# Kernel optimization log

Measured on AMD Instinct MI355X. Metric: run time of the kernel, lower is better.

The kernel has to match this reference:

```python
import jax, jax.numpy as jnp
import numpy as np

E = 5          # number of experts / candidate encoders
NSUB = 13      # subband axis from x.reshape([B, 13, -1])


def _complex_corr_mean(y, y_):
    # y: [E, B, 13, F] (interleaved re/im), y_: [B, 13, F]
    ai, aj = y[..., 0::2], y[..., 1::2]        # [E,B,13,F/2]
    bi, bj = y_[..., 0::2], y_[..., 1::2]      # [B,13,F/2]
    i = (ai * bi + aj * bj).sum(-1)            # [E,B,13]
    j = (ai * bj - aj * bi).sum(-1)            # [E,B,13]
    c = i * i + j * j                          # |<a, conj(b)>|^2 per subband
    return c.mean(-1)                          # [E,B]


def setup_inputs() -> dict:
    key = jax.random.key(0)
    k = jax.random.split(key, 5)
    B, F, D = 4096, 9984, 512
    return {
        "x": jax.random.normal(k[0], (B, F), dtype=jnp.float32),
        "W_enc": jax.random.normal(k[1], (E, F, D), dtype=jnp.float32) * 0.02,
        "b_enc": jnp.zeros((E, D), dtype=jnp.float32),
        "W_dec": jax.random.normal(k[2], (E, D, F), dtype=jnp.float32) * 0.02,
        "b_dec": jnp.zeros((E, F), dtype=jnp.float32),
    }


def reference(x, W_enc, b_enc, W_dec, b_dec):
    B = x.shape[0]
    # per-expert encode: out[e] = encoder_e(x) -> latent code [E, B, D]
    out = jnp.einsum("bf,efd->ebd", x, W_enc) + b_enc[:, None, :]
    # per-expert decode: y[e] = decoder_e(out[e]) -> reconstruction [E, B, F]
    y = jnp.einsum("ebd,edf->ebf", out, W_dec) + b_dec[:, None, :]
    y = y.reshape(E, B, NSUB, -1)
    y_ = x.reshape(B, NSUB, -1)
    scores = _complex_corr_mean(y, y_)         # [E, B]
    idx = jnp.argmax(scores, axis=0)           # [B] best expert per sample
    # batch_gather: pick the winning expert's latent per sample
    sel = out[idx, jnp.arange(B)]              # [B, D]
    return sel
```

## Files before the change

### kernel.cpp

```cpp
#include <hip/hip_runtime.h>

#define E_ 5
#define B_ 4096
#define F_ 9984
#define D_ 512
#define NSUB_ 13
#define SUBW_ 768

typedef _Float16 f16;
typedef __attribute__((ext_vector_type(4))) _Float16 f16x4;
typedef __attribute__((ext_vector_type(8))) _Float16 f16x8;
typedef __attribute__((ext_vector_type(16))) float f32x16;

#define BK 32
#define PLANE_H 4096
#define BUF_H   16384

#define MFMA(a, b, c) __builtin_amdgcn_mfma_f32_32x32x16_f16((a), (b), (c), 0, 0, 0)

__device__ __forceinline__ void gload16(const f16* g, f16* l) {
    __builtin_amdgcn_global_load_lds(
        (const __attribute__((address_space(1))) void*)g,
        (__attribute__((address_space(3))) void*)l, 16, 0, 0);
}

template<int BOFF>
__device__ __forceinline__ void computeK5(const f16* lds,
        int aA0s0, int aA0s1, int aA1s0, int aA1s1,
        int aB0s0, int aB0s1, int aB1s0, int aB1s1,
        f32x16 accm[2][2], f32x16 accx[2][2]) {
    #pragma unroll
    for (int sub = 0; sub < 2; ++sub) {
        const int oA0 = sub ? aA0s1 : aA0s0;
        const int oA1 = sub ? aA1s1 : aA1s0;
        const int oB0 = sub ? aB0s1 : aB0s0;
        const int oB1 = sub ? aB1s1 : aB1s0;
        f16x8 ah0 = *(const f16x8*)(lds + BOFF + 0*PLANE_H + oA0);
        f16x8 ah1 = *(const f16x8*)(lds + BOFF + 0*PLANE_H + oA1);
        f16x8 al0 = *(const f16x8*)(lds + BOFF + 1*PLANE_H + oA0);
        f16x8 al1 = *(const f16x8*)(lds + BOFF + 1*PLANE_H + oA1);
        f16x8 bh0 = *(const f16x8*)(lds + BOFF + 2*PLANE_H + oB0);
        f16x8 bh1 = *(const f16x8*)(lds + BOFF + 2*PLANE_H + oB1);
        f16x8 bl0 = *(const f16x8*)(lds + BOFF + 3*PLANE_H + oB0);
        f16x8 bl1 = *(const f16x8*)(lds + BOFF + 3*PLANE_H + oB1);
        accm[0][0] = MFMA(ah0, bh0, accm[0][0]);
        accm[0][1] = MFMA(ah0, bh1, accm[0][1]);
        accm[1][0] = MFMA(ah1, bh0, accm[1][0]);
        accm[1][1] = MFMA(ah1, bh1, accm[1][1]);
        accx[0][0] = MFMA(ah0, bl0, accx[0][0]);
        accx[0][0] = MFMA(al0, bh0, accx[0][0]);
        accx[0][1] = MFMA(ah0, bl1, accx[0][1]);
        accx[0][1] = MFMA(al0, bh1, accx[0][1]);
        accx[1][0] = MFMA(ah1, bl0, accx[1][0]);
        accx[1][0] = MFMA(al1, bh0, accx[1][0]);
        accx[1][1] = MFMA(ah1, bl1, accx[1][1]);
        accx[1][1] = MFMA(al1, bh1, accx[1][1]);
    }
}

__device__ __forceinline__ void gemm_core5(
    const f16* __restrict__ Ah, const f16* __restrict__ Al, int sA,
    const f16* __restrict__ Bh, const f16* __restrict__ Bl, int sB,
    int nk, f16* lds, int t, int wm, int wn, int l31, int g,
    f32x16 accm[2][2], f32x16 accx[2][2])
{
    const int lane = t & 63, wid = t >> 6;
    const int lrow = lane >> 2, lch = lane & 3;
    const f16* gp = (wid == 0) ? Ah : (wid == 1) ? Al : (wid == 2) ? Bh : Bl;
    const int gs = (wid < 2) ? sA : sB;

    const f16* gps[8];
    int ldoff[8];
    #pragma unroll
    for (int s = 0; s < 8; ++s) {
        const int row = s * 16 + lrow;
        gps[s] = gp + (size_t)row * gs + ((lch ^ ((row >> 1) & 3)) << 3);
        ldoff[s] = wid * PLANE_H + s * (16 * BK);
    }

    const int rowA0 = wm + l31,      rowA1 = wm + 32 + l31;
    const int rowB0 = wn + l31,      rowB1 = wn + 32 + l31;
    const int kA0 = (rowA0 >> 1) & 3, kA1 = (rowA1 >> 1) & 3;
    const int kB0 = (rowB0 >> 1) & 3, kB1 = (rowB1 >> 1) & 3;
    const int aA0s0 = rowA0 * BK + (((0 + g) ^ kA0) << 3);
    const int aA0s1 = rowA0 * BK + (((2 + g) ^ kA0) << 3);
    const int aA1s0 = rowA1 * BK + (((0 + g) ^ kA1) << 3);
    const int aA1s1 = rowA1 * BK + (((2 + g) ^ kA1) << 3);
    const int aB0s0 = rowB0 * BK + (((0 + g) ^ kB0) << 3);
    const int aB0s1 = rowB0 * BK + (((2 + g) ^ kB0) << 3);
    const int aB1s0 = rowB1 * BK + (((0 + g) ^ kB1) << 3);
    const int aB1s1 = rowB1 * BK + (((2 + g) ^ kB1) << 3);

    #pragma unroll
    for (int s = 0; s < 8; ++s)
        gload16(gps[s], lds + ldoff[s]);
    #pragma unroll
    for (int s = 0; s < 8; ++s)
        gps[s] += BK;

    for (int kt = 0; kt < nk; kt += 2) {
        #pragma unroll
        for (int s = 0; s < 8; ++s)
            gload16(gps[s], lds + BUF_H + ldoff[s]);
        #pragma unroll
        for (int s = 0; s < 8; ++s)
            gps[s] += BK;
        asm volatile("s_waitcnt vmcnt(8)" ::: "memory");
        __builtin_amdgcn_s_barrier();
        __builtin_amdgcn_sched_barrier(0);
        __builtin_amdgcn_s_setprio(1);
        computeK5<0>(lds, aA0s0, aA0s1, aA1s0, aA1s1,
                     aB0s0, aB0s1, aB1s0, aB1s1, accm, accx);
        __builtin_amdgcn_s_setprio(0);
        __builtin_amdgcn_sched_barrier(0);
        __builtin_amdgcn_s_barrier();
        __builtin_amdgcn_sched_barrier(0);

        if (kt + 2 < nk) {
            #pragma unroll
            for (int s = 0; s < 8; ++s)
                gload16(gps[s], lds + ldoff[s]);
            #pragma unroll
            for (int s = 0; s < 8; ++s)
                gps[s] += BK;
            asm volatile("s_waitcnt vmcnt(8)" ::: "memory");
        } else {
            asm volatile("s_waitcnt vmcnt(0)" ::: "memory");
        }
        __builtin_amdgcn_s_barrier();
        __builtin_amdgcn_sched_barrier(0);
        __builtin_amdgcn_s_setprio(1);
        computeK5<BUF_H>(lds, aA0s0, aA0s1, aA1s0, aA1s1,
                         aB0s0, aB0s1, aB1s0, aB1s1, accm, accx);
        __builtin_amdgcn_s_setprio(0);
        __builtin_amdgcn_sched_barrier(0);
        __builtin_amdgcn_s_barrier();
        __builtin_amdgcn_sched_barrier(0);
    }
}

__global__ __launch_bounds__(256) void split_x(const float* __restrict__ x,
                                               f16* __restrict__ xhi, f16* __restrict__ xlo) {
    size_t i = ((size_t)blockIdx.x * 256 + threadIdx.x) * 4;
    float4 v = *(const float4*)&x[i];
    float vv[4] = {v.x, v.y, v.z, v.w};
    f16x4 h, l;
    #pragma unroll
    for (int k = 0; k < 4; ++k) {
        f16 hh = (f16)vv[k];
        h[k] = hh;
        l[k] = (f16)((vv[k] - (float)hh) * 2048.0f);
    }
    *(f16x4*)&xhi[i] = h;
    *(f16x4*)&xlo[i] = l;
}

__global__ __launch_bounds__(256) void splitT_W(const float* __restrict__ W,
                                                f16* __restrict__ Thi, f16* __restrict__ Tlo,
                                                int R, int C) {
    __shared__ float tile[64][65];
    const int rt = blockIdx.x, ct = blockIdx.y, e = blockIdx.z;
    const int t = threadIdx.x;
    const int r0 = rt * 64, c0 = ct * 64;
    const int tr = t >> 4, tc4 = (t & 15) * 4;
    const float* Wp = W + (size_t)e * R * C;
    #pragma unroll
    for (int p = 0; p < 4; ++p) {
        float4 v = *(const float4*)&Wp[(size_t)(r0 + tr + p*16) * C + c0 + tc4];
        tile[tr + p*16][tc4 + 0] = v.x;
        tile[tr + p*16][tc4 + 1] = v.y;
        tile[tr + p*16][tc4 + 2] = v.z;
        tile[tr + p*16][tc4 + 3] = v.w;
    }
    __syncthreads();
    f16* Th = Thi + (size_t)e * R * C;
    f16* Tl = Tlo + (size_t)e * R * C;
    #pragma unroll
    for (int p = 0; p < 4; ++p) {
        const int cr = tr + p*16;
        f16x4 h, l;
        #pragma unroll
        for (int k = 0; k < 4; ++k) {
            float v = tile[tc4 + k][cr] * 64.0f;
            f16 hh = (f16)v;
            h[k] = hh;
            l[k] = (f16)((v - (float)hh) * 2048.0f);
        }
        size_t off = (size_t)(c0 + cr) * R + r0 + tc4;
        *(f16x4*)&Th[off] = h;
        *(f16x4*)&Tl[off] = l;
    }
}

__global__ __launch_bounds__(256, 2) void mm_enc2(
    const f16* __restrict__ xhi, const f16* __restrict__ xlo,
    const f16* __restrict__ wthi, const f16* __restrict__ wtlo,
    const float* __restrict__ bias, int Kloc,
    f16* __restrict__ outHi, f16* __restrict__ outLo)
{
    __shared__ f16 lds[2 * BUF_H];
    const int gx = blockIdx.x;
    const int de = gx % 20;
    const int bl = gx / 20;
    const int bt = blockIdx.y * 4 + bl;
    const int ks = blockIdx.z;
    const int dt = de & 3, e = de >> 2;
    const int koff = ks * Kloc;
    const int t = threadIdx.x, lane = t & 63, l31 = lane & 31, g = lane >> 5, wid = t >> 6;
    const int wm = (wid >> 1) * 64, wn = (wid & 1) * 64;
    const f16* Ah = xhi + (size_t)bt * 128 * F_ + koff;
    const f16* Al = xlo + (size_t)bt * 128 * F_ + koff;
    const f16* Bh = wthi + ((size_t)e * D_ + dt * 128) * F_ + koff;
    const f16* Bl = wtlo + ((size_t)e * D_ + dt * 128) * F_ + koff;
    f32x16 accm[2][2] = {}, accx[2][2] = {};
    gemm_core5(Ah, Al, F_, Bh, Bl, F_, Kloc / BK, lds, t, wm, wn, l31, g, accm, accx);

    f16* oH = outHi + (size_t)ks * E_ * B_ * D_;
    f16* oL = outLo + (size_t)ks * E_ * B_ * D_;
    #pragma unroll
    for (int fn = 0; fn < 2; ++fn) {
        const int d = dt * 128 + wn + fn * 32 + l31;
        const float be = bias ? bias[e * D_ + d] : 0.0f;
        #pragma unroll
        for (int fm = 0; fm < 2; ++fm) {
            #pragma unroll
            for (int r = 0; r < 16; ++r) {
                float v = (accm[fm][fn][r] + accx[fm][fn][r] * (1.0f/2048.0f)) * (1.0f/64.0f) + be;
                int brow = bt * 128 + wm + fm * 32 + (r & 3) + 8 * (r >> 2) + 4 * g;
                size_t off = ((size_t)e * B_ + brow) * D_ + d;
                f16 h = (f16)v;
                oH[off] = h;
                oL[off] = (f16)((v - (float)h) * 2048.0f);
            }
        }
    }
}

__global__ __launch_bounds__(256) void combine_k(
    const f16* __restrict__ pH, const f16* __restrict__ pL,
    const float* __restrict__ b_enc,
    f16* __restrict__ oH, f16* __restrict__ oL)
{
    const size_t NP = (size_t)E_ * B_ * D_;
    size_t i = ((size_t)blockIdx.x * 256 + threadIdx.x) * 8;
    f16x8 h0 = *(const f16x8*)(pH + i);
    f16x8 l0 = *(const f16x8*)(pL + i);
    f16x8 h1 = *(const f16x8*)(pH + NP + i);
    f16x8 l1 = *(const f16x8*)(pL + NP + i);
    const int d = (int)(i % D_);
    const int e = (int)(i / ((size_t)B_ * D_));
    f16x8 oh, ol;
    #pragma unroll
    for (int k = 0; k < 8; ++k) {
        float v = (float)h0[k] + (float)l0[k] * (1.0f/2048.0f)
                + (float)h1[k] + (float)l1[k] * (1.0f/2048.0f)
                + b_enc[e * D_ + d + k];
        f16 hh = (f16)v;
        oh[k] = hh;
        ol[k] = (f16)((v - (float)hh) * 2048.0f);
    }
    *(f16x8*)&oH[i] = oh;
    *(f16x8*)&oL[i] = ol;
}

__global__ __launch_bounds__(256, 2) void mm_dec2(
    const f16* __restrict__ wthi, const f16* __restrict__ wtlo,
    const f16* __restrict__ ohi, const f16* __restrict__ olo,
    const float* __restrict__ b_dec, const float* __restrict__ x,
    float* __restrict__ ijbuf)
{
    __shared__ __align__(16) f16 lds[33280];
    const int bt = blockIdx.x;
    const int ft = blockIdx.y;
    const int se = blockIdx.z;
    const int e = se % 5, s = se / 5;
    const int t = threadIdx.x, lane = t & 63, l31 = lane & 31, g = lane >> 5, wid = t >> 6;
    const int wm = (wid >> 1) * 64, wn = (wid & 1) * 64;
    const int f0blk = s * SUBW_ + ft * 128;
    const f16* Ah = wthi + ((size_t)e * F_ + f0blk) * D_;
    const f16* Al = wtlo + ((size_t)e * F_ + f0blk) * D_;
    const f16* Bh = ohi + ((size_t)e * B_ + bt * 128) * D_;
    const f16* Bl = olo + ((size_t)e * B_ + bt * 128) * D_;
    f32x16 accm[2][2] = {}, accx[2][2] = {};
    gemm_core5(Ah, Al, D_, Bh, Bl, D_, D_ / BK, lds, t, wm, wn, l31, g, accm, accx);

    float* xs = (float*)lds;
    {
        const int fb = (t & 31) * 4;
        const int h  = fb >> 6, fl = fb & 63;
        float* dst0 = xs + h * (128 * 65) + fl;
        const float* src = &x[(size_t)(bt * 128 + (t >> 5)) * F_ + f0blk + fb];
        #pragma unroll
        for (int it = 0; it < 16; ++it) {
            const int b = (t >> 5) + it * 8;
            float4 v = *(const float4*)(src + (size_t)it * 8 * F_);
            float* dst = dst0 + b * 65;
            dst[0] = v.x; dst[1] = v.y; dst[2] = v.z; dst[3] = v.w;
        }
    }
    __syncthreads();

    const float* xsw = xs + (wm >> 6) * (128 * 65);
    float ia[2] = {0.f, 0.f}, ja[2] = {0.f, 0.f};
    #pragma unroll
    for (int fm = 0; fm < 2; ++fm) {
        #pragma unroll
        for (int q = 0; q < 8; ++q) {
            const int r = q * 2;
            const int fl = fm * 32 + (r & 3) + 8 * (r >> 2) + 4 * g;
            const int fg = f0blk + wm + fl;
            const float2 bd = *(const float2*)&b_dec[(size_t)e * F_ + fg];
            #pragma unroll
            for (int fn = 0; fn < 2; ++fn) {
                const int bl_ = wn + fn * 32 + l31;
                const float x0 = xsw[bl_ * 65 + fl];
                const float x1 = xsw[bl_ * 65 + fl + 1];
                float y0 = (accm[fm][fn][r]     + accx[fm][fn][r]     * (1.0f/2048.0f)) * (1.0f/64.0f) + bd.x;
                float y1 = (accm[fm][fn][r + 1] + accx[fm][fn][r + 1] * (1.0f/2048.0f)) * (1.0f/64.0f) + bd.y;
                ia[fn] += y0 * x0 + y1 * x1;
                ja[fn] += y0 * x1 - y1 * x0;
            }
        }
    }
    #pragma unroll
    for (int fn = 0; fn < 2; ++fn) {
        ia[fn] += __shfl_xor(ia[fn], 32, 64);
        ja[fn] += __shfl_xor(ja[fn], 32, 64);
    }
    __syncthreads();
    float* red = (float*)lds;
    const int wr = wid >> 1, wc = wid & 1;
    if (wr == 0 && lane < 32) {
        #pragma unroll
        for (int fn = 0; fn < 2; ++fn) {
            red[(wc * 64 + fn * 32 + l31) * 2 + 0] = ia[fn];
            red[(wc * 64 + fn * 32 + l31) * 2 + 1] = ja[fn];
        }
    }
    __syncthreads();
    if (wr == 1 && lane < 32) {
        #pragma unroll
        for (int fn = 0; fn < 2; ++fn) {
            float gi = ia[fn] + red[(wc * 64 + fn * 32 + l31) * 2 + 0];
            float gj = ja[fn] + red[(wc * 64 + fn * 32 + l31) * 2 + 1];
            int b = bt * 128 + wc * 64 + fn * 32 + l31;
            size_t base = (((size_t)(e * NSUB_ + s)) * 6 + ft) * 2;
            ijbuf[(base + 0) * B_ + b] = gi;
            ijbuf[(base + 1) * B_ + b] = gj;
        }
    }
}

__global__ __launch_bounds__(256) void argmax2(const float* __restrict__ ijbuf, int* __restrict__ idx) {
    int b = blockIdx.x * 256 + threadIdx.x;
    float best = -1.0f; int bi = 0;
    for (int e = 0; e < E_; ++e) {
        float sc = 0.f;
        for (int s = 0; s < NSUB_; ++s) {
            float ii = 0.f, jj = 0.f;
            #pragma unroll
            for (int ft = 0; ft < 6; ++ft) {
                size_t base = (((size_t)(e * NSUB_ + s)) * 6 + ft) * 2;
                ii += ijbuf[base * B_ + b];
                jj += ijbuf[(base + 1) * B_ + b];
            }
            sc += ii * ii + jj * jj;
        }
        if (sc > best) { best = sc; bi = e; }
    }
    idx[b] = bi;
}

__global__ __launch_bounds__(256) void gather2(const f16* __restrict__ outHi, const f16* __restrict__ outLo,
                                               const int* __restrict__ idx, float* __restrict__ sel) {
    int tg = blockIdx.x * 256 + threadIdx.x;
    int b = tg >> 7, dq = (tg & 127) * 4;
    int e = idx[b];
    size_t off = ((size_t)e * B_ + b) * D_ + dq;
    f16x4 h = *(const f16x4*)&outHi[off];
    f16x4 l = *(const f16x4*)&outLo[off];
    float4 o;
    o.x = (float)h[0] + (float)l[0] * (1.0f/2048.0f);
    o.y = (float)h[1] + (float)l[1] * (1.0f/2048.0f);
    o.z = (float)h[2] + (float)l[2] * (1.0f/2048.0f);
    o.w = (float)h[3] + (float)l[3] * (1.0f/2048.0f);
    *(float4*)&sel[(size_t)b * D_ + dq] = o;
}

__global__ __launch_bounds__(256) void enc_gemm(const float* __restrict__ x,
                                                const float* __restrict__ W_enc,
                                                const float* __restrict__ b_enc,
                                                float* __restrict__ out)
{
    __shared__ float As[16][68];
    __shared__ float Bs[16][68];
    const int btile = blockIdx.x;
    const int en    = blockIdx.y;
    const int e  = en >> 3;
    const int n0 = (en & 7) * 64;
    const int b0 = btile * 64;
    const int tid = threadIdx.x;
    const int tx = tid & 15, ty = tid >> 4;
    const float* Wp = W_enc + (size_t)e * F_ * D_;
    const int arow = tid >> 2;
    const int ac4  = (tid & 3) * 4;
    const int bk   = tid >> 4;
    const int bn   = (tid & 15) * 4;
    float acc[4][4] = {};
    for (int k0 = 0; k0 < F_; k0 += 16) {
        float4 av = *(const float4*)&x[(size_t)(b0 + arow) * F_ + k0 + ac4];
        As[ac4 + 0][arow] = av.x; As[ac4 + 1][arow] = av.y;
        As[ac4 + 2][arow] = av.z; As[ac4 + 3][arow] = av.w;
        float4 bv = *(const float4*)&Wp[(size_t)(k0 + bk) * D_ + n0 + bn];
        *(float4*)&Bs[bk][bn] = bv;
        __syncthreads();
        #pragma unroll
        for (int k = 0; k < 16; ++k) {
            float4 a = *(const float4*)&As[k][ty * 4];
            float4 b = *(const float4*)&Bs[k][tx * 4];
            float ar[4] = {a.x, a.y, a.z, a.w};
            float br[4] = {b.x, b.y, b.z, b.w};
            #pragma unroll
            for (int r = 0; r < 4; ++r)
                #pragma unroll
                for (int c = 0; c < 4; ++c)
                    acc[r][c] += ar[r] * br[c];
        }
        __syncthreads();
    }
    float4 be = *(const float4*)&b_enc[e * D_ + n0 + tx * 4];
    #pragma unroll
    for (int r = 0; r < 4; ++r) {
        int b = b0 + ty * 4 + r;
        float4 o;
        o.x = acc[r][0] + be.x; o.y = acc[r][1] + be.y;
        o.z = acc[r][2] + be.z; o.w = acc[r][3] + be.w;
        *(float4*)&out[((size_t)e * B_ + b) * D_ + n0 + tx * 4] = o;
    }
}

__global__ __launch_bounds__(256) void dec_score(const float* __restrict__ out,
                                                 const float* __restrict__ W_dec,
                                                 const float* __restrict__ b_dec,
                                                 const float* __restrict__ x,
                                                 float* __restrict__ cbuf)
{
    __shared__ float As[16][68];
    __shared__ float Bs[16][68];
    const int btile = blockIdx.x;
    const int es    = blockIdx.y;
    const int e = es / 13;
    const int s = es % 13;
    const int b0 = btile * 64;
    const int fbase = s * SUBW_;
    const int tid = threadIdx.x;
    const int tx = tid & 15, ty = tid >> 4;
    const float* Ap = out   + (size_t)e * B_ * D_;
    const float* Wp = W_dec + (size_t)e * D_ * F_;
    const int arow = tid >> 2;
    const int ac4  = (tid & 3) * 4;
    const int bk   = tid >> 4;
    const int bn   = (tid & 15) * 4;
    float ip[4] = {}, jp[4] = {};
    for (int u = 0; u < 12; ++u) {
        const int f0 = fbase + u * 64;
        float acc[4][4] = {};
        for (int k0 = 0; k0 < D_; k0 += 16) {
            float4 av = *(const float4*)&Ap[(size_t)(b0 + arow) * D_ + k0 + ac4];
            As[ac4 + 0][arow] = av.x; As[ac4 + 1][arow] = av.y;
            As[ac4 + 2][arow] = av.z; As[ac4 + 3][arow] = av.w;
            float4 bv = *(const float4*)&Wp[(size_t)(k0 + bk) * F_ + f0 + bn];
            *(float4*)&Bs[bk][bn] = bv;
            __syncthreads();
            #pragma unroll
            for (int k = 0; k < 16; ++k) {
                float4 a = *(const float4*)&As[k][ty * 4];
                float4 b = *(const float4*)&Bs[k][tx * 4];
                float ar[4] = {a.x, a.y, a.z, a.w};
                float br[4] = {b.x, b.y, b.z, b.w};
                #pragma unroll
                for (int r = 0; r < 4; ++r)
                    #pragma unroll
                    for (int c = 0; c < 4; ++c)
                        acc[r][c] += ar[r] * br[c];
            }
            __syncthreads();
        }
        float4 bd = *(const float4*)&b_dec[(size_t)e * F_ + f0 + tx * 4];
        #pragma unroll
        for (int r = 0; r < 4; ++r) {
            int b = b0 + ty * 4 + r;
            float4 xv = *(const float4*)&x[(size_t)b * F_ + f0 + tx * 4];
            float y0 = acc[r][0] + bd.x;
            float y1 = acc[r][1] + bd.y;
            float y2 = acc[r][2] + bd.z;
            float y3 = acc[r][3] + bd.w;
            ip[r] += y0 * xv.x + y1 * xv.y + y2 * xv.z + y3 * xv.w;
            jp[r] += y0 * xv.y - y1 * xv.x + y2 * xv.w - y3 * xv.z;
        }
    }
    #pragma unroll
    for (int r = 0; r < 4; ++r) {
        float iv = ip[r], jv = jp[r];
        #pragma unroll
        for (int m = 1; m < 16; m <<= 1) {
            iv += __shfl_xor(iv, m, 64);
            jv += __shfl_xor(jv, m, 64);
        }
        if (tx == 0) {
            int b = b0 + ty * 4 + r;
            cbuf[((size_t)e * B_ + b) * NSUB_ + s] = iv * iv + jv * jv;
        }
    }
}

__global__ __launch_bounds__(256) void argmax_k(const float* __restrict__ cbuf,
                                                int* __restrict__ idx)
{
    int b = blockIdx.x * blockDim.x + threadIdx.x;
    if (b >= B_) return;
    float best = -1e30f;
    int bi = 0;
    for (int e = 0; e < E_; ++e) {
        float ssum = 0.f;
        #pragma unroll
        for (int s = 0; s < NSUB_; ++s)
            ssum += cbuf[((size_t)e * B_ + b) * NSUB_ + s];
        if (ssum > best) { best = ssum; bi = e; }
    }
    idx[b] = bi;
}

__global__ __launch_bounds__(256) void gather_k(const float* __restrict__ out,
                                                const int* __restrict__ idx,
                                                float* __restrict__ sel)
{
    int t = blockIdx.x * blockDim.x + threadIdx.x;
    int b = t >> 7;
    int c = (t & 127) * 4;
    int e = idx[b];
    *(float4*)&sel[(size_t)b * D_ + c] =
        *(const float4*)&out[((size_t)e * B_ + b) * D_ + c];
}

extern "C" void kernel_launch(void* const* d_in, const int* in_sizes, int n_in,
                              void* d_out, int out_size, void* d_ws, size_t ws_size,
                              hipStream_t stream)
{
    const float* x     = (const float*)d_in[0];
    const float* W_enc = (const float*)d_in[1];
    const float* b_enc = (const float*)d_in[2];
    const float* W_dec = (const float*)d_in[3];
    const float* b_dec = (const float*)d_in[4];
    float* sel = (float*)d_out;

    const size_t szXplane = (size_t)B_ * F_ * sizeof(f16);
    const size_t szWplane = (size_t)E_ * F_ * D_ * sizeof(f16);
    const size_t szOplane = (size_t)E_ * B_ * D_ * sizeof(f16);
    const size_t szIJ     = (size_t)E_ * NSUB_ * 6 * 2 * B_ * sizeof(float);
    const size_t need      = 2*szXplane + 2*szWplane + 2*szOplane + szIJ + (size_t)B_*4;
    const size_t needSplit = need + 4*szOplane;

    if (ws_size >= need) {
        char* p = (char*)d_ws;
        f16* xhi  = (f16*)p; p += szXplane;
        f16* xlo  = (f16*)p; p += szXplane;
        f16* wthi = (f16*)p; p += szWplane;
        f16* wtlo = (f16*)p; p += szWplane;
        f16* ohi  = (f16*)p; p += szOplane;
        f16* olo  = (f16*)p; p += szOplane;
        float* ij = (float*)p; p += szIJ;
        int* idx  = (int*)p; p += (size_t)B_*4;

        split_x<<<39936, 256, 0, stream>>>(x, xhi, xlo);
        splitT_W<<<dim3(F_/64, D_/64, E_), 256, 0, stream>>>(W_enc, wthi, wtlo, F_, D_);

        if (ws_size >= needSplit) {
            f16* pH = (f16*)p; p += 2*szOplane;
            f16* pL = (f16*)p;
            mm_enc2<<<dim3(80, 8, 2), 256, 0, stream>>>(xhi, xlo, wthi, wtlo,
                                                        nullptr, F_/2, pH, pL);
            combine_k<<<(E_*B_*D_)/(8*256), 256, 0, stream>>>(pH, pL, b_enc, ohi, olo);
        } else {
            mm_enc2<<<dim3(80, 8, 1), 256, 0, stream>>>(xhi, xlo, wthi, wtlo,
                                                        b_enc, F_, ohi, olo);
        }
        splitT_W<<<dim3(D_/64, F_/64, E_), 256, 0, stream>>>(W_dec, wthi, wtlo, D_, F_);
        mm_dec2<<<dim3(32, 6, 65), 256, 0, stream>>>(wthi, wtlo, ohi, olo, b_dec, x, ij);
        argmax2<<<16, 256, 0, stream>>>(ij, idx);
        gather2<<<2048, 256, 0, stream>>>(ohi, olo, idx, sel);
    } else {
        float* out  = (float*)d_ws;
        float* cbuf = out + (size_t)E_ * B_ * D_;
        int*   idx  = (int*)(cbuf + (size_t)E_ * B_ * NSUB_);
        enc_gemm <<<dim3(64, 40), 256, 0, stream>>>(x, W_enc, b_enc, out);
        dec_score<<<dim3(64, 65), 256, 0, stream>>>(out, W_dec, b_dec, x, cbuf);
        argmax_k <<<dim3(B_ / 256), 256, 0, stream>>>(cbuf, idx);
        gather_k <<<dim3(B_ * D_ / 4 / 256), 256, 0, stream>>>(out, idx, sel);
    }
}
```

Baseline: 1.709 ms.

## Replace double-buffered K=32 GEMM pipeline with four-stage K=16 ring buffer

The shared GEMM core moves from a two-buffer scheme with a K tile of 32 to a four-slot ring of K=16 tiles, keeping three stages of global-to-LDS loads in flight and using one barrier per step instead of two. The XOR swizzle and per-lane load mapping are adapted to the narrower 16-element rows. The goal is to hide global memory latency better and cut barrier overhead per MFMA group. The cost is fewer MFMAs per synchronization step, and a __syncthreads is added before the decoder reuses LDS for its epilogue.

```diff
diff --git a/kernel.cpp b/kernel.cpp
--- a/kernel.cpp
+++ b/kernel.cpp
@@ -12,9 +12,9 @@
 typedef __attribute__((ext_vector_type(8))) _Float16 f16x8;
 typedef __attribute__((ext_vector_type(16))) float f32x16;
 
-#define BK 32
-#define PLANE_H 4096
-#define BUF_H   16384
+#define BK16 16
+#define PL16 2048
+#define BUF16 8192
 
 #define MFMA(a, b, c) __builtin_amdgcn_mfma_f32_32x32x16_f16((a), (b), (c), 0, 0, 0)
 
@@ -25,118 +25,97 @@
 }
 
 template<int BOFF>
-__device__ __forceinline__ void computeK5(const f16* lds,
-        int aA0s0, int aA0s1, int aA1s0, int aA1s1,
-        int aB0s0, int aB0s1, int aB1s0, int aB1s1,
+__device__ __forceinline__ void computeK16(const f16* lds,
+        int aA0, int aA1, int aB0, int aB1,
         f32x16 accm[2][2], f32x16 accx[2][2]) {
-    #pragma unroll
-    for (int sub = 0; sub < 2; ++sub) {
-        const int oA0 = sub ? aA0s1 : aA0s0;
-        const int oA1 = sub ? aA1s1 : aA1s0;
-        const int oB0 = sub ? aB0s1 : aB0s0;
-        const int oB1 = sub ? aB1s1 : aB1s0;
-        f16x8 ah0 = *(const f16x8*)(lds + BOFF + 0*PLANE_H + oA0);
-        f16x8 ah1 = *(const f16x8*)(lds + BOFF + 0*PLANE_H + oA1);
-        f16x8 al0 = *(const f16x8*)(lds + BOFF + 1*PLANE_H + oA0);
-        f16x8 al1 = *(const f16x8*)(lds + BOFF + 1*PLANE_H + oA1);
-        f16x8 bh0 = *(const f16x8*)(lds + BOFF + 2*PLANE_H + oB0);
-        f16x8 bh1 = *(const f16x8*)(lds + BOFF + 2*PLANE_H + oB1);
-        f16x8 bl0 = *(const f16x8*)(lds + BOFF + 3*PLANE_H + oB0);
-        f16x8 bl1 = *(const f16x8*)(lds + BOFF + 3*PLANE_H + oB1);
-        accm[0][0] = MFMA(ah0, bh0, accm[0][0]);
-        accm[0][1] = MFMA(ah0, bh1, accm[0][1]);
-        accm[1][0] = MFMA(ah1, bh0, accm[1][0]);
-        accm[1][1] = MFMA(ah1, bh1, accm[1][1]);
-        accx[0][0] = MFMA(ah0, bl0, accx[0][0]);
-        accx[0][0] = MFMA(al0, bh0, accx[0][0]);
-        accx[0][1] = MFMA(ah0, bl1, accx[0][1]);
-        accx[0][1] = MFMA(al0, bh1, accx[0][1]);
-        accx[1][0] = MFMA(ah1, bl0, accx[1][0]);
-        accx[1][0] = MFMA(al1, bh0, accx[1][0]);
-        accx[1][1] = MFMA(ah1, bl1, accx[1][1]);
-        accx[1][1] = MFMA(al1, bh1, accx[1][1]);
-    }
-}
-
-__device__ __forceinline__ void gemm_core5(
+    f16x8 ah0 = *(const f16x8*)(lds + BOFF + 0*PL16 + aA0);
+    f16x8 ah1 = *(const f16x8*)(lds + BOFF + 0*PL16 + aA1);
+    f16x8 al0 = *(const f16x8*)(lds + BOFF + 1*PL16 + aA0);
+    f16x8 al1 = *(const f16x8*)(lds + BOFF + 1*PL16 + aA1);
+    f16x8 bh0 = *(const f16x8*)(lds + BOFF + 2*PL16 + aB0);
+    f16x8 bh1 = *(const f16x8*)(lds + BOFF + 2*PL16 + aB1);
+    f16x8 bl0 = *(const f16x8*)(lds + BOFF + 3*PL16 + aB0);
+    f16x8 bl1 = *(const f16x8*)(lds + BOFF + 3*PL16 + aB1);
+    accm[0][0] = MFMA(ah0, bh0, accm[0][0]);
+    accm[0][1] = MFMA(ah0, bh1, accm[0][1]);
+    accm[1][0] = MFMA(ah1, bh0, accm[1][0]);
+    accm[1][1] = MFMA(ah1, bh1, accm[1][1]);
+    accx[0][0] = MFMA(ah0, bl0, accx[0][0]);
+    accx[0][0] = MFMA(al0, bh0, accx[0][0]);
+    accx[0][1] = MFMA(ah0, bl1, accx[0][1]);
+    accx[0][1] = MFMA(al0, bh1, accx[0][1]);
+    accx[1][0] = MFMA(ah1, bl0, accx[1][0]);
+    accx[1][0] = MFMA(al1, bh0, accx[1][0]);
+    accx[1][1] = MFMA(ah1, bl1, accx[1][1]);
+    accx[1][1] = MFMA(al1, bh1, accx[1][1]);
+}
+
+__device__ __forceinline__ void gemm_core6(
     const f16* __restrict__ Ah, const f16* __restrict__ Al, int sA,
     const f16* __restrict__ Bh, const f16* __restrict__ Bl, int sB,
-    int nk, f16* lds, int t, int wm, int wn, int l31, int g,
+    int ns, f16* lds, int t, int wm, int wn, int l31, int g,
     f32x16 accm[2][2], f32x16 accx[2][2])
 {
     const int lane = t & 63, wid = t >> 6;
-    const int lrow = lane >> 2, lch = lane & 3;
+    const int lrow = lane >> 1, lch = lane & 1;
     const f16* gp = (wid == 0) ? Ah : (wid == 1) ? Al : (wid == 2) ? Bh : Bl;
     const int gs = (wid < 2) ? sA : sB;
 
-    const f16* gps[8];
-    int ldoff[8];
-    #pragma unroll
-    for (int s = 0; s < 8; ++s) {
-        const int row = s * 16 + lrow;
-        gps[s] = gp + (size_t)row * gs + ((lch ^ ((row >> 1) & 3)) << 3);
-        ldoff[s] = wid * PLANE_H + s * (16 * BK);
+    const f16* gps[4];
+    int ldoff[4];
+    #pragma unroll
+    for (int j = 0; j < 4; ++j) {
+        const int row = j * 32 + lrow;
+        gps[j] = gp + (size_t)row * gs + ((lch ^ ((row >> 1) & 1)) << 3);
+        ldoff[j] = wid * PL16 + j * 512;
     }
 
     const int rowA0 = wm + l31,      rowA1 = wm + 32 + l31;
     const int rowB0 = wn + l31,      rowB1 = wn + 32 + l31;
-    const int kA0 = (rowA0 >> 1) & 3, kA1 = (rowA1 >> 1) & 3;
-    const int kB0 = (rowB0 >> 1) & 3, kB1 = (rowB1 >> 1) & 3;
-    const int aA0s0 = rowA0 * BK + (((0 + g) ^ kA0) << 3);
-    const int aA0s1 = rowA0 * BK + (((2 + g) ^ kA0) << 3);
-    const int aA1s0 = rowA1 * BK + (((0 + g) ^ kA1) << 3);
-    const int aA1s1 = rowA1 * BK + (((2 + g) ^ kA1) << 3);
-    const int aB0s0 = rowB0 * BK + (((0 + g) ^ kB0) << 3);
-    const int aB0s1 = rowB0 * BK + (((2 + g) ^ kB0) << 3);
-    const int aB1s0 = rowB1 * BK + (((0 + g) ^ kB1) << 3);
-    const int aB1s1 = rowB1 * BK + (((2 + g) ^ kB1) << 3);
-
-    #pragma unroll
-    for (int s = 0; s < 8; ++s)
-        gload16(gps[s], lds + ldoff[s]);
-    #pragma unroll
-    for (int s = 0; s < 8; ++s)
-        gps[s] += BK;
-
-    for (int kt = 0; kt < nk; kt += 2) {
-        #pragma unroll
-        for (int s = 0; s < 8; ++s)
-            gload16(gps[s], lds + BUF_H + ldoff[s]);
-        #pragma unroll
-        for (int s = 0; s < 8; ++s)
-            gps[s] += BK;
-        asm volatile("s_waitcnt vmcnt(8)" ::: "memory");
-        __builtin_amdgcn_s_barrier();
-        __builtin_amdgcn_sched_barrier(0);
-        __builtin_amdgcn_s_setprio(1);
-        computeK5<0>(lds, aA0s0, aA0s1, aA1s0, aA1s1,
-                     aB0s0, aB0s1, aB1s0, aB1s1, accm, accx);
-        __builtin_amdgcn_s_setprio(0);
-        __builtin_amdgcn_sched_barrier(0);
-        __builtin_amdgcn_s_barrier();
-        __builtin_amdgcn_sched_barrier(0);
-
-        if (kt + 2 < nk) {
-            #pragma unroll
-            for (int s = 0; s < 8; ++s)
-                gload16(gps[s], lds + ldoff[s]);
-            #pragma unroll
-            for (int s = 0; s < 8; ++s)
-                gps[s] += BK;
-            asm volatile("s_waitcnt vmcnt(8)" ::: "memory");
-        } else {
-            asm volatile("s_waitcnt vmcnt(0)" ::: "memory");
-        }
-        __builtin_amdgcn_s_barrier();
-        __builtin_amdgcn_sched_barrier(0);
-        __builtin_amdgcn_s_setprio(1);
-        computeK5<BUF_H>(lds, aA0s0, aA0s1, aA1s0, aA1s1,
-                         aB0s0, aB0s1, aB1s0, aB1s1, accm, accx);
-        __builtin_amdgcn_s_setprio(0);
-        __builtin_amdgcn_sched_barrier(0);
-        __builtin_amdgcn_s_barrier();
-        __builtin_amdgcn_sched_barrier(0);
-    }
+    const int aA0 = rowA0 * BK16 + ((g ^ ((rowA0 >> 1) & 1)) << 3);
+    const int aA1 = rowA1 * BK16 + ((g ^ ((rowA1 >> 1) & 1)) << 3);
+    const int aB0 = rowB0 * BK16 + ((g ^ ((rowB0 >> 1) & 1)) << 3);
+    const int aB1 = rowB1 * BK16 + ((g ^ ((rowB1 >> 1) & 1)) << 3);
+
+    #pragma unroll
+    for (int b = 0; b < 3; ++b)
+        #pragma unroll
+        for (int j = 0; j < 4; ++j)
+            gload16(gps[j] + b * BK16, lds + b * BUF16 + ldoff[j]);
+    #pragma unroll
+    for (int j = 0; j < 4; ++j)
+        gps[j] += 3 * BK16;
+
+#define BODY6(KIDX)                                                          \
+    {                                                                        \
+        const int s_ = S + (KIDX);                                           \
+        const int ahead_ = ns - 1 - s_;                                      \
+        if (ahead_ >= 2)      asm volatile("s_waitcnt vmcnt(8)" ::: "memory");\
+        else if (ahead_ == 1) asm volatile("s_waitcnt vmcnt(4)" ::: "memory");\
+        else                  asm volatile("s_waitcnt vmcnt(0)" ::: "memory");\
+        __builtin_amdgcn_s_barrier();                                        \
+        __builtin_amdgcn_sched_barrier(0);                                   \
+        if (s_ + 3 < ns) {                                                   \
+            _Pragma("unroll")                                                \
+            for (int j = 0; j < 4; ++j)                                      \
+                gload16(gps[j], lds + (((KIDX) + 3) & 3) * BUF16 + ldoff[j]);\
+            _Pragma("unroll")                                                \
+            for (int j = 0; j < 4; ++j)                                      \
+                gps[j] += BK16;                                              \
+        }                                                                    \
+        __builtin_amdgcn_s_setprio(1);                                       \
+        computeK16<(KIDX) * BUF16>(lds, aA0, aA1, aB0, aB1, accm, accx);     \
+        __builtin_amdgcn_s_setprio(0);                                       \
+        __builtin_amdgcn_sched_barrier(0);                                   \
+    }
+
+    for (int S = 0; S < ns; S += 4) {
+        BODY6(0)
+        BODY6(1)
+        BODY6(2)
+        BODY6(3)
+    }
+#undef BODY6
 }
 
 __global__ __launch_bounds__(256) void split_x(const float* __restrict__ x,
@@ -198,7 +177,7 @@
     const float* __restrict__ bias, int Kloc,
     f16* __restrict__ outHi, f16* __restrict__ outLo)
 {
-    __shared__ f16 lds[2 * BUF_H];
+    __shared__ __align__(16) f16 lds[4 * BUF16];
     const int gx = blockIdx.x;
     const int de = gx % 20;
     const int bl = gx / 20;
@@ -213,7 +192,7 @@
     const f16* Bh = wthi + ((size_t)e * D_ + dt * 128) * F_ + koff;
     const f16* Bl = wtlo + ((size_t)e * D_ + dt * 128) * F_ + koff;
     f32x16 accm[2][2] = {}, accx[2][2] = {};
-    gemm_core5(Ah, Al, F_, Bh, Bl, F_, Kloc / BK, lds, t, wm, wn, l31, g, accm, accx);
+    gemm_core6(Ah, Al, F_, Bh, Bl, F_, Kloc / BK16, lds, t, wm, wn, l31, g, accm, accx);
 
     f16* oH = outHi + (size_t)ks * E_ * B_ * D_;
     f16* oL = outLo + (size_t)ks * E_ * B_ * D_;
@@ -282,7 +261,8 @@
     const f16* Bh = ohi + ((size_t)e * B_ + bt * 128) * D_;
     const f16* Bl = olo + ((size_t)e * B_ + bt * 128) * D_;
     f32x16 accm[2][2] = {}, accx[2][2] = {};
-    gemm_core5(Ah, Al, D_, Bh, Bl, D_, D_ / BK, lds, t, wm, wn, l31, g, accm, accx);
+    gemm_core6(Ah, Al, D_, Bh, Bl, D_, D_ / BK16, lds, t, wm, wn, l31, g, accm, accx);
+    __syncthreads();
 
     float* xs = (float*)lds;
     {
```

After: 2.067 ms. 1.21x slower.
